# Performance work log

Measured on AMD Instinct MI355X. Metric: run time of the kernel, lower is better.

The kernel has to match this reference:

```python
import jax, jax.numpy as jnp
import numpy as np

C = 128          # multiplicity of 0e and 1o irreps
N = 16384        # number of tokens / points
SQRT2 = 2.0 ** 0.5
SQRT3 = 3.0 ** 0.5


def _tensor_square(s, v):
    """Per-channel symmetric tensor square of (1x0e + 1x1o).
    s: (N,C) scalars, v: (N,C,3) vectors.
    Returns ss:(N,C) 0e, sv:(N,C,3) 1o, vv0:(N,C) 0e, q:(N,C,5) 2e."""
    ss = s * s
    sv = SQRT2 * s[..., None] * v
    vv0 = jnp.sum(v * v, axis=-1) / SQRT3
    x, y, z = v[..., 0], v[..., 1], v[..., 2]
    q = jnp.stack([
        SQRT3 * x * y,
        SQRT3 * y * z,
        (2.0 * z * z - x * x - y * y) / 2.0,
        SQRT3 * x * z,
        SQRT3 * (x * x - y * y) / 2.0,
    ], axis=-1)
    return ss, sv, vv0, q


def _block(s, v, w1, w2, w0, wv):
    """_SelfInteractionBlock: tensor_square + concat/regroup + invariant-gated MLP + equivariant Linear."""
    ss, sv, vv0, q = _tensor_square(s, v)
    # regrouped features: 3C x 0e, 2C x 1o, C x 2e
    sc = jnp.concatenate([s, ss, vv0], axis=-1)            # (N, 3C)
    vec = jnp.concatenate([v, sv], axis=1)                 # (N, 2C, 3)
    # gate MLP on invariants (fan-in normalized, silu hidden)
    h = jax.nn.silu(sc @ w1 / jnp.sqrt(jnp.float32(sc.shape[-1])))
    g = h @ w2 / jnp.sqrt(jnp.float32(h.shape[-1]))        # (N, 6C) one gate per irrep
    g_s = g[:, :3 * C]
    g_v = g[:, 3 * C:5 * C]
    # (2e gates multiply q, which is dropped by the Linear to Cx0e+Cx1o)
    sc = sc * g_s
    vec = vec * g_v[..., None]
    # block-diagonal equivariant Linear -> C x 0e + C x 1o
    out_s = sc @ w0 / jnp.sqrt(jnp.float32(sc.shape[-1]))                      # (N, C)
    out_v = jnp.einsum('nmd,mc->ncd', vec, wv) / jnp.sqrt(jnp.float32(vec.shape[1]))  # (N, C, 3)
    return out_s, out_v


def _eq_layernorm(s, v, g0, g1, eps=1e-6):
    mu = jnp.mean(s, axis=-1, keepdims=True)
    sd = jnp.sqrt(jnp.mean((s - mu) ** 2, axis=-1, keepdims=True) + eps)
    s = (s - mu) / sd * g0
    rms = jnp.sqrt(jnp.mean(v * v, axis=(1, 2), keepdims=True) + eps)
    v = v / rms * g1[None, :, None]
    return s, v


def setup_inputs() -> dict:
    key = jax.random.key(0)
    ks = jax.random.split(key, 6)
    x = jax.random.normal(ks[0], (N, 4 * C), dtype=jnp.float32)
    mlp_w1 = jax.random.normal(ks[1], (2, 3 * C, 3 * C), dtype=jnp.float32)
    mlp_w2 = jax.random.normal(ks[2], (2, 3 * C, 6 * C), dtype=jnp.float32)
    lin_w0 = jax.random.normal(ks[3], (2, 3 * C, C), dtype=jnp.float32)
    lin_w1 = jax.random.normal(ks[4], (2, 2 * C, C), dtype=jnp.float32)
    ln_g0 = jnp.ones((C,), dtype=jnp.float32)
    ln_g1 = jnp.ones((C,), dtype=jnp.float32)
    return {"x": x, "mlp_w1": mlp_w1, "mlp_w2": mlp_w2,
            "lin_w0": lin_w0, "lin_w1": lin_w1, "ln_g0": ln_g0, "ln_g1": ln_g1}


def reference(x, mlp_w1, mlp_w2, lin_w0, lin_w1, ln_g0, ln_g1):
    n = x.shape[0]
    s = x[:, :C]                         # C x 0e
    v = x[:, C:].reshape(n, C, 3)        # C x 1o
    n_layers = mlp_w1.shape[0]
    for i in range(n_layers):
        ds, dv = _block(s, v, mlp_w1[i], mlp_w2[i], lin_w0[i], lin_w1[i])
        s = s + ds   # residual
        v = v + dv
        if i != n_layers - 1:  # norm on all but last layer (norm_last=False)
            s, v = _eq_layernorm(s, v, ln_g0, ln_g1)
    return jnp.concatenate([s, v.reshape(n, 3 * C)], axis=-1)
```

## Files before the change

### kernel.cpp

```cpp
#include <hip/hip_runtime.h>


typedef _Float16 half8 __attribute__((ext_vector_type(8)));
typedef float floatx4 __attribute__((ext_vector_type(4)));

static inline int cdiv_h(int a, int b){ return (a + b - 1) / b; }


__device__ __forceinline__ void stage16(const char* gaddr, char* lds_base){
  __builtin_amdgcn_global_load_lds((const __attribute__((address_space(1))) unsigned int*)gaddr,
                                   (__attribute__((address_space(3))) unsigned int*)lds_base,
                                   16, 0, 0);
}

__device__ __forceinline__ float wave_sum64(float x){
  #pragma unroll
  for (int m = 32; m; m >>= 1) x += __shfl_xor(x, m, 64);
  return x;
}

__device__ __forceinline__ void split_store(_Float16* p0, _Float16* p1, float v){
  _Float16 hi = (_Float16)v;
  *p0 = hi;
  *p1 = (_Float16)(v - (float)hi);
}

__device__ __forceinline__ unsigned int pack_split(float v){
  union { _Float16 h[2]; unsigned int u; } pk;
  _Float16 hi = (_Float16)v;
  pk.h[0] = hi;
  pk.h[1] = (_Float16)(v - (float)hi);
  return pk.u;
}

__device__ __forceinline__ void unzip16(uint4 p, uint2& hi, uint2& lo){
  hi.x = (p.x & 0xffffu) | (p.y << 16);
  hi.y = (p.z & 0xffffu) | (p.w << 16);
  lo.x = (p.x >> 16) | (p.y & 0xffff0000u);
  lo.y = (p.z >> 16) | (p.w & 0xffff0000u);
}

__device__ __forceinline__ void remap_xcd(int id, int nx, int ny, int& x, int& y){
  if (ny & 7){ x = id % nx; y = id / nx; return; }
  int xcd = id & 7, q = id >> 3, t = q / nx;
  x = q - t*nx; y = xcd + (t << 3);
}

__global__ __launch_bounds__(256) void prep_all(const float* __restrict__ w1,
                                                const float* __restrict__ w2,
                                                const float* __restrict__ w0,
                                                const float* __restrict__ wv,
                                                _Float16* __restrict__ W){
  const int PER_L = 475136;
  int idx = blockIdx.x*256 + threadIdx.x;
  if (idx >= 2*PER_L) return;
  int l = idx / PER_L;
  int r = idx - l*PER_L;
  const float RS384 = 0.051031036307982884f;
  _Float16* WL = W + (size_t)l*950272;
  const float* src; _Float16* dst; int K, ldw, col, k; float scale;
  if (r < 147456){
    src = w1 + (size_t)l*147456; dst = WL;            K = 384; ldw = 384; scale = RS384;
    col = r / 384; k = r - col*384;
  } else if (r < 393216){
    r -= 147456;
    src = w2 + (size_t)l*294912; dst = WL + 294912;   K = 384; ldw = 768; scale = RS384;
    col = r / 384; k = r - col*384;
  } else if (r < 442368){
    r -= 393216;
    src = w0 + (size_t)l*49152;  dst = WL + 786432;   K = 384; ldw = 128; scale = RS384;
    col = r / 384; k = r - col*384;
  } else {
    r -= 442368;
    src = wv + (size_t)l*32768;  dst = WL + 884736;   K = 256; ldw = 128; scale = 0.0625f;
    col = r / 256; k = r - col*256;
  }
  float v = src[(size_t)k*ldw + col] * scale;
  _Float16 hi = (_Float16)v;
  _Float16 lo = (_Float16)(v - (float)hi);
  size_t b = (size_t)col*2*K + k;
  dst[b]     = hi;
  dst[b + K] = lo;
}

__global__ __launch_bounds__(256) void e0_fused(const float* __restrict__ x,
                                                float* __restrict__ S,
                                                float* __restrict__ V,
                                                _Float16* __restrict__ A1,
                                                int row0){
  __shared__ alignas(16) float lx[4][512];
  const int n0 = blockIdx.x*4;
  const int tid = threadIdx.x;
  const float4* xs = (const float4*)(x + (size_t)(row0 + n0)*512);
  float4* ls = (float4*)(&lx[0][0]);
  ls[tid]       = xs[tid];
  ls[tid + 256] = xs[tid + 256];
  __syncthreads();
  const int w = tid >> 6, lane = tid & 63;
  const int n = n0 + w;
  const float* row = &lx[w][0];
  #pragma unroll
  for (int h = 0; h < 2; ++h){
    int ch = h*64 + lane;
    float s = row[ch];
    S[(size_t)n*128 + ch] = s;
    float vv = 0.f;
    #pragma unroll
    for (int d = 0; d < 3; ++d){
      float vd = row[128 + ch*3 + d];
      V[((size_t)n*3 + d)*128 + ch] = vd;
      vv += vd*vd;
    }
    float vals[3] = { s, s*s, vv * 0.5773502691896258f };
    #pragma unroll
    for (int q = 0; q < 3; ++q){
      size_t b = (size_t)n*768 + q*128 + ch;
      split_store(&A1[b], &A1[b + 384], vals[q]);
    }
  }
}

__global__ __launch_bounds__(256) void e3_fin(float* __restrict__ S, float* __restrict__ V,
                                              const float* __restrict__ OS, const float* __restrict__ OV,
                                              const float* __restrict__ g0, const float* __restrict__ g1,
                                              float* __restrict__ out, _Float16* __restrict__ A1,
                                              int row0, int doln){
  int n = blockIdx.x*4 + (threadIdx.x >> 6);
  int lane = threadIdx.x & 63;
  size_t sb = (size_t)n*128;
  size_t vb = (size_t)n*384;
  float s0 = S[sb + lane]      + OS[sb + lane];
  float s1 = S[sb + 64 + lane] + OS[sb + 64 + lane];
  float v[6];
  #pragma unroll
  for (int k = 0; k < 6; ++k) v[k] = V[vb + k*64 + lane] + OV[vb + k*64 + lane];

  if (doln){
    float mu = wave_sum64(s0 + s1) * (1.0f/128.0f);
    float d0 = s0 - mu, d1 = s1 - mu;
    float var = wave_sum64(d0*d0 + d1*d1) * (1.0f/128.0f);
    float sd = sqrtf(var + 1e-6f);
    float vvsum = 0.f;
    #pragma unroll
    for (int k = 0; k < 6; ++k) vvsum += v[k]*v[k];
    float rms = sqrtf(wave_sum64(vvsum) * (1.0f/384.0f) + 1e-6f);
    float s0n = d0 / sd * g0[lane];
    float s1n = d1 / sd * g0[64 + lane];
    S[sb + lane]      = s0n;
    S[sb + 64 + lane] = s1n;
    float vn[6];
    #pragma unroll
    for (int k = 0; k < 6; ++k){
      int j = k*64 + lane;
      vn[k] = v[k] / rms * g1[j & 127];
      V[vb + j] = vn[k];
    }
    float vv_a = vn[0]*vn[0] + vn[2]*vn[2] + vn[4]*vn[4];
    float vv_b = vn[1]*vn[1] + vn[3]*vn[3] + vn[5]*vn[5];
    float va[3] = { s0n, s0n*s0n, vv_a * 0.5773502691896258f };
    float vbv[3]= { s1n, s1n*s1n, vv_b * 0.5773502691896258f };
    #pragma unroll
    for (int q = 0; q < 3; ++q){
      size_t ba = (size_t)n*768 + q*128 + lane;
      split_store(&A1[ba], &A1[ba + 384], va[q]);
      size_t bb = ba + 64;
      split_store(&A1[bb], &A1[bb + 384], vbv[q]);
    }
  } else {
    size_t ob = (size_t)(row0 + n)*512;
    out[ob + lane]      = s0;
    out[ob + 64 + lane] = s1;
    #pragma unroll
    for (int k = 0; k < 6; ++k){
      int j = k*64 + lane;
      int d = j >> 7, ch = j & 127;
      out[ob + 128 + ch*3 + d] = v[k];
    }
  }
}

__device__ __forceinline__ void gemm_mainloop(const _Float16* __restrict__ A,
                                              const _Float16* __restrict__ BT,
                                              int lda, int kbase, int m0, int c0,
                                              _Float16 (&ls)[2][12288],
                                              floatx4 (&acc)[4][2]){
  const int nsc  = kbase >> 5;
  const int ldbt = 2*kbase;
  const int tid  = threadIdx.x;
  const int wave = tid >> 6, lane = tid & 63;
  const int wm = wave & 1, wn = wave >> 1;
  const int r = lane & 15, kg = lane >> 4;
  const int slot = kg ^ ((r >> 1) & 3);

  auto stage = [&](int c, int buf){
    const int ka = c << 5;
    char* lb = (char*)(&ls[buf][0]);
    #pragma unroll
    for (int p = 0; p < 2; ++p){
      const int lbase = wave*1024 + p*4096;
      const int off = lbase + lane*16;
      const int row = off >> 6;
      const int bir = (off & 63) ^ (((off >> 7) & 3) << 4);
      const char* gah = (const char*)A + (((size_t)(m0 + row))*lda + ka)*2 + bir;
      stage16(gah, lb + lbase);
      const char* gal = (const char*)A + (((size_t)(m0 + row))*lda + kbase + ka)*2 + bir;
      stage16(gal, lb + 8192 + lbase);
    }
    {
      const int lbase = wave*1024;
      const int off = lbase + lane*16;
      const int row = off >> 6;
      const int bir = (off & 63) ^ (((off >> 7) & 3) << 4);
      const char* gbh = (const char*)BT + (((size_t)(c0 + row))*ldbt + ka)*2 + bir;
      stage16(gbh, lb + 16384 + lbase);
      const char* gbl = (const char*)BT + (((size_t)(c0 + row))*ldbt + kbase + ka)*2 + bir;
      stage16(gbl, lb + 20480 + lbase);
    }
  };

  stage(0, 0);
  for (int c = 0; c < nsc; ++c){
    __syncthreads();
    if (c + 1 < nsc) stage(c + 1, (c + 1) & 1);
    const char* base = (const char*)&ls[c & 1][0];
    half8 ah[4], al[4], bh[2], bl[2];
    #pragma unroll
    for (int mt = 0; mt < 4; ++mt){
      const int ro = (wm*64 + mt*16 + r)*64 + slot*16;
      ah[mt] = *(const half8*)(base + ro);
      al[mt] = *(const half8*)(base + 8192 + ro);
    }
    #pragma unroll
    for (int nt = 0; nt < 2; ++nt){
      const int ro = (wn*32 + nt*16 + r)*64 + slot*16;
      bh[nt] = *(const half8*)(base + 16384 + ro);
      bl[nt] = *(const half8*)(base + 20480 + ro);
    }
    #pragma unroll
    for (int mt = 0; mt < 4; ++mt)
      #pragma unroll
      for (int nt = 0; nt < 2; ++nt)
        acc[mt][nt] = __builtin_amdgcn_mfma_f32_16x16x32_f16(ah[mt], bh[nt], acc[mt][nt], 0, 0, 0);
    #pragma unroll
    for (int mt = 0; mt < 4; ++mt)
      #pragma unroll
      for (int nt = 0; nt < 2; ++nt)
        acc[mt][nt] = __builtin_amdgcn_mfma_f32_16x16x32_f16(ah[mt], bl[nt], acc[mt][nt], 0, 0, 0);
    #pragma unroll
    for (int mt = 0; mt < 4; ++mt)
      #pragma unroll
      for (int nt = 0; nt < 2; ++nt)
        acc[mt][nt] = __builtin_amdgcn_mfma_f32_16x16x32_f16(al[mt], bh[nt], acc[mt][nt], 0, 0, 0);
  }
}

template<int MODE>
__global__ __launch_bounds__(256, 3) void gemm_split(const _Float16* __restrict__ A,
                                                     const _Float16* __restrict__ BT,
                                                     _Float16* __restrict__ OUT,
                                                     const float* __restrict__ S,
                                                     const float* __restrict__ V,
                                                     _Float16* __restrict__ A1g,
                                                     _Float16* __restrict__ A4,
                                                     int lda, int kbase, int nx, int ny){
  __shared__ alignas(16) _Float16 ls[2][12288];
  int bx, by; remap_xcd(blockIdx.x, nx, ny, bx, by);
  const int c0 = bx << 6, m0 = by << 7;
  floatx4 acc[4][2];
  #pragma unroll
  for (int i = 0; i < 4; ++i)
    #pragma unroll
    for (int j = 0; j < 2; ++j) acc[i][j] = (floatx4){0.f, 0.f, 0.f, 0.f};

  gemm_mainloop(A, BT, lda, kbase, m0, c0, ls, acc);

  const int tid = threadIdx.x;
  const int wave = tid >> 6, lane = tid & 63;
  const int wm = wave & 1, wn = wave >> 1;
  const int r = lane & 15, kg = lane >> 4;
  char* scr = (char*)&ls[0][0];

  if (MODE == 1){
    #pragma unroll
    for (int h = 0; h < 2; ++h){
      __syncthreads();
      if (wm == h){
        #pragma unroll
        for (int mt = 0; mt < 4; ++mt)
          #pragma unroll
          for (int nt = 0; nt < 2; ++nt)
            #pragma unroll
            for (int i = 0; i < 4; ++i){
              int rl = mt*16 + kg*4 + i;
              int cl = wn*32 + nt*16 + r;
              int pc = cl ^ (kg << 4);
              float g = acc[mt][nt][i];
              float hh = g / (1.0f + __expf(-g));
              *(unsigned int*)(scr + rl*256 + pc*4) = pack_split(hh);
            }
      }
      __syncthreads();
      #pragma unroll 1
      for (int j = 0; j < 4; ++j){
        int lin = j*256 + tid, rl = lin >> 4, seg = lin & 15;
        int cs = seg ^ (((rl >> 2) & 3) << 2);
        uint4 p = *(const uint4*)(scr + rl*256 + cs*16);
        uint2 hi, lo; unzip16(p, hi, lo);
        _Float16* rowp = OUT + (size_t)(m0 + h*64 + rl)*768 + c0 + seg*4;
        *(uint2*)rowp         = hi;
        *(uint2*)(rowp + 384) = lo;
      }
    }
  } else if (c0 < 384){
    #pragma unroll
    for (int h = 0; h < 2; ++h){
      __syncthreads();
      #pragma unroll 1
      for (int j = 0; j < 2; ++j){
        int lin = j*256 + tid, rl = lin >> 3, seg = lin & 7;
        int cs = seg ^ (((rl >> 2) & 3) << 1);
        const _Float16* gp = A1g + (size_t)(m0 + h*64 + rl)*768 + c0 + seg*8;
        *(float4*)(scr + rl*128 + cs*16)        = *(const float4*)gp;
        *(float4*)(scr + 8192 + rl*128 + cs*16) = *(const float4*)(gp + 384);
      }
      __syncthreads();
      if (wm == h){
        #pragma unroll
        for (int mt = 0; mt < 4; ++mt)
          #pragma unroll
          for (int nt = 0; nt < 2; ++nt)
            #pragma unroll
            for (int i = 0; i < 4; ++i){
              int rl = mt*16 + kg*4 + i;
              int cl = wn*32 + nt*16 + r;
              int pc = cl ^ (kg << 4);
              _Float16* phi = (_Float16*)scr + rl*64 + pc;
              _Float16* plo = (_Float16*)(scr + 8192) + rl*64 + pc;
              float sc = (float)*phi + (float)*plo;
              split_store(phi, plo, sc * acc[mt][nt][i]);
            }
      }
      __syncthreads();
      #pragma unroll 1
      for (int j = 0; j < 2; ++j){
        int lin = j*256 + tid, rl = lin >> 3, seg = lin & 7;
        int cs = seg ^ (((rl >> 2) & 3) << 1);
        _Float16* gp = A1g + (size_t)(m0 + h*64 + rl)*768 + c0 + seg*8;
        *(float4*)gp         = *(const float4*)(scr + rl*128 + cs*16);
        *(float4*)(gp + 384) = *(const float4*)(scr + 8192 + rl*128 + cs*16);
      }
    }
  } else {
    const int mm0 = c0 - 384;
    const int ch0 = mm0 & 127;
    if (mm0 >= 128){
      #pragma unroll
      for (int mt = 0; mt < 4; ++mt)
        #pragma unroll
        for (int nt = 0; nt < 2; ++nt)
          #pragma unroll
          for (int i = 0; i < 4; ++i){
            int row = m0 + wm*64 + mt*16 + kg*4 + i;
            int cl  = wn*32 + nt*16 + r;
            acc[mt][nt][i] *= 1.4142135623730951f * S[(size_t)row*128 + ch0 + cl];
          }
    }
    for (int d = 0; d < 3; ++d){
      #pragma unroll
      for (int h = 0; h < 2; ++h){
        __syncthreads();
        #pragma unroll 1
        for (int j = 0; j < 4; ++j){
          int lin = j*256 + tid, rl = lin >> 4, seg = lin & 15;
          int cs = seg ^ (((rl >> 2) & 3) << 2);
          *(float4*)(scr + rl*256 + cs*16) =
            *(const float4*)(V + ((size_t)(m0 + h*64 + rl)*3 + d)*128 + ch0 + seg*4);
        }
        __syncthreads();
        if (wm == h){
          #pragma unroll
          for (int mt = 0; mt < 4; ++mt)
            #pragma unroll
            for (int nt = 0; nt < 2; ++nt)
              #pragma unroll
              for (int i = 0; i < 4; ++i){
                int rl = mt*16 + kg*4 + i;
                int cl = wn*32 + nt*16 + r;
                int pc = cl ^ (kg << 4);
                float* pw = (float*)(scr + rl*256) + pc;
                *(unsigned int*)pw = pack_split(*pw * acc[mt][nt][i]);
              }
        }
        __syncthreads();
        #pragma unroll 1
        for (int j = 0; j < 4; ++j){
          int lin = j*256 + tid, rl = lin >> 4, seg = lin & 15;
          int cs = seg ^ (((rl >> 2) & 3) << 2);
          uint4 p = *(const uint4*)(scr + rl*256 + cs*16);
          uint2 hi, lo; unzip16(p, hi, lo);
          _Float16* rowp = A4 + ((size_t)(m0 + h*64 + rl)*3 + d)*512 + mm0 + seg*4;
          *(uint2*)rowp         = hi;
          *(uint2*)(rowp + 256) = lo;
        }
      }
    }
  }
}

__global__ __launch_bounds__(256, 3) void gemm_pair(const _Float16* __restrict__ Aa,
                                                    const _Float16* __restrict__ Ba,
                                                    float* __restrict__ Ca, int ny0,
                                                    const _Float16* __restrict__ Ab,
                                                    const _Float16* __restrict__ Bb,
                                                    float* __restrict__ Cb, int ny1){
  __shared__ alignas(16) _Float16 ls[2][12288];
  const _Float16 *A, *BT; float* C; int lda, kbase, bx, by;
  const int id = blockIdx.x;
  if (id < 2*ny0){
    remap_xcd(id, 2, ny0, bx, by);
    A = Aa; BT = Ba; C = Ca; lda = 768; kbase = 384;
  } else {
    remap_xcd(id - 2*ny0, 2, ny1, bx, by);
    A = Ab; BT = Bb; C = Cb; lda = 512; kbase = 256;
  }
  const int c0 = bx << 6, m0 = by << 7;
  floatx4 acc[4][2];
  #pragma unroll
  for (int i = 0; i < 4; ++i)
    #pragma unroll
    for (int j = 0; j < 2; ++j) acc[i][j] = (floatx4){0.f, 0.f, 0.f, 0.f};

  gemm_mainloop(A, BT, lda, kbase, m0, c0, ls, acc);

  const int wave = threadIdx.x >> 6, lane = threadIdx.x & 63;
  const int wm = wave & 1, wn = wave >> 1;
  const int r = lane & 15, kg = lane >> 4;
  #pragma unroll
  for (int mt = 0; mt < 4; ++mt)
    #pragma unroll
    for (int nt = 0; nt < 2; ++nt)
      #pragma unroll
      for (int i = 0; i < 4; ++i){
        const int row = m0 + wm*64 + mt*16 + kg*4 + i;
        const int col = c0 + wn*32 + nt*16 + r;
        C[(size_t)row*128 + col] = acc[mt][nt][i];
      }
}


extern "C" void kernel_launch(void* const* d_in, const int* in_sizes, int n_in,
                              void* d_out, int out_size, void* d_ws, size_t ws_size,
                              hipStream_t stream){
  const float* x  = (const float*)d_in[0];
  const float* w1 = (const float*)d_in[1];
  const float* w2 = (const float*)d_in[2];
  const float* w0 = (const float*)d_in[3];
  const float* wv = (const float*)d_in[4];
  const float* g0 = (const float*)d_in[5];
  const float* g1 = (const float*)d_in[6];
  float* out = (float*)d_out;
  const int N = in_sizes[0] / 512;

  const size_t HL = 950272;
  _Float16* W = (_Float16*)d_ws;
  const size_t wbytes = 2*HL*2;

  int cnum = 128;
  for (int cc = 1; cc <= 128; cc <<= 1){
    size_t need = wbytes + (size_t)(N/cc)*10240;
    if (need <= ws_size){ cnum = cc; break; }
  }
  const int R = N / cnum;
  const int ny = R / 128;

  char* p = (char*)d_ws + wbytes;
  float*    Sst = (float*)p;     p += (size_t)R*512;
  float*    Vst = (float*)p;     p += (size_t)R*1536;
  _Float16* A1  = (_Float16*)p;  p += (size_t)R*1536;
  _Float16* A2  = (_Float16*)p;  p += (size_t)R*1536;
  _Float16* A4  = (_Float16*)p;  p += (size_t)R*3072;
  float*    OS  = (float*)p;     p += (size_t)R*512;
  float*    OV  = (float*)p;     p += (size_t)R*1536;

  prep_all<<<cdiv_h(2*475136,256),256,0,stream>>>(w1, w2, w0, wv, W);

  for (int chk = 0; chk < cnum; ++chk){
    const int row0 = chk*R;
    e0_fused<<<R/4,256,0,stream>>>(x, Sst, Vst, A1, row0);
    for (int l = 0; l < 2; ++l){
      _Float16* W1p = W + (size_t)l*HL;
      _Float16* W2p = W1p + 294912;
      _Float16* W0p = W1p + 786432;
      _Float16* WVp = W1p + 884736;
      gemm_split<1><<<6*ny,256,0,stream>>>(A1, W1p, A2,
          nullptr, nullptr, nullptr, nullptr, 768, 384, 6, ny);
      gemm_split<2><<<10*ny,256,0,stream>>>(A2, W2p, nullptr,
          Sst, Vst, A1, A4, 768, 384, 10, ny);
      gemm_pair<<<8*ny,256,0,stream>>>(A1, W0p, OS, ny, A4, WVp, OV, 3*ny);
      e3_fin<<<R/4,256,0,stream>>>(Sst, Vst, OS, OV, g0, g1, out, A1, row0, (l == 0) ? 1 : 0);
    }
  }
}
```

Baseline: 357.4 us.

## Load GEMM operands directly from global memory into registers, dropping LDS staging

Replaces the double-buffered global_load_lds staging of A/B tiles in shared memory with direct per-lane 16-byte global loads into MFMA operand registers. This removes LDS traffic and the per-iteration __syncthreads. The epilogue scratch shrinks to 16 KB, and launch bounds go from 3 to 4 blocks per SM for more occupancy. The cost is that each wave now reloads data the other waves also use, so there is no intra-block reuse and global/L2 traffic rises. With no prefetch, load latency is exposed at every k-step.

```diff
diff --git a/kernel.cpp b/kernel.cpp
--- a/kernel.cpp
+++ b/kernel.cpp
@@ -6,12 +6,6 @@
 
 static inline int cdiv_h(int a, int b){ return (a + b - 1) / b; }
 
-
-__device__ __forceinline__ void stage16(const char* gaddr, char* lds_base){
-  __builtin_amdgcn_global_load_lds((const __attribute__((address_space(1))) unsigned int*)gaddr,
-                                   (__attribute__((address_space(3))) unsigned int*)lds_base,
-                                   16, 0, 0);
-}
 
 __device__ __forceinline__ float wave_sum64(float x){
   #pragma unroll
@@ -182,60 +176,30 @@
 __device__ __forceinline__ void gemm_mainloop(const _Float16* __restrict__ A,
                                               const _Float16* __restrict__ BT,
                                               int lda, int kbase, int m0, int c0,
-                                              _Float16 (&ls)[2][12288],
                                               floatx4 (&acc)[4][2]){
-  const int nsc  = kbase >> 5;
+  const int nsc = kbase >> 5;
   const int ldbt = 2*kbase;
-  const int tid  = threadIdx.x;
+  const int tid = threadIdx.x;
   const int wave = tid >> 6, lane = tid & 63;
   const int wm = wave & 1, wn = wave >> 1;
   const int r = lane & 15, kg = lane >> 4;
-  const int slot = kg ^ ((r >> 1) & 3);
-
-  auto stage = [&](int c, int buf){
-    const int ka = c << 5;
-    char* lb = (char*)(&ls[buf][0]);
-    #pragma unroll
-    for (int p = 0; p < 2; ++p){
-      const int lbase = wave*1024 + p*4096;
-      const int off = lbase + lane*16;
-      const int row = off >> 6;
-      const int bir = (off & 63) ^ (((off >> 7) & 3) << 4);
-      const char* gah = (const char*)A + (((size_t)(m0 + row))*lda + ka)*2 + bir;
-      stage16(gah, lb + lbase);
-      const char* gal = (const char*)A + (((size_t)(m0 + row))*lda + kbase + ka)*2 + bir;
-      stage16(gal, lb + 8192 + lbase);
-    }
-    {
-      const int lbase = wave*1024;
-      const int off = lbase + lane*16;
-      const int row = off >> 6;
-      const int bir = (off & 63) ^ (((off >> 7) & 3) << 4);
-      const char* gbh = (const char*)BT + (((size_t)(c0 + row))*ldbt + ka)*2 + bir;
-      stage16(gbh, lb + 16384 + lbase);
-      const char* gbl = (const char*)BT + (((size_t)(c0 + row))*ldbt + kbase + ka)*2 + bir;
-      stage16(gbl, lb + 20480 + lbase);
-    }
-  };
-
-  stage(0, 0);
+
+  const _Float16* pa0 = A + (size_t)(m0 + wm*64 +  0 + r)*lda + kg*8;
+  const _Float16* pa1 = A + (size_t)(m0 + wm*64 + 16 + r)*lda + kg*8;
+  const _Float16* pa2 = A + (size_t)(m0 + wm*64 + 32 + r)*lda + kg*8;
+  const _Float16* pa3 = A + (size_t)(m0 + wm*64 + 48 + r)*lda + kg*8;
+  const _Float16* pb0 = BT + (size_t)(c0 + wn*32 +  0 + r)*ldbt + kg*8;
+  const _Float16* pb1 = BT + (size_t)(c0 + wn*32 + 16 + r)*ldbt + kg*8;
+
   for (int c = 0; c < nsc; ++c){
-    __syncthreads();
-    if (c + 1 < nsc) stage(c + 1, (c + 1) & 1);
-    const char* base = (const char*)&ls[c & 1][0];
     half8 ah[4], al[4], bh[2], bl[2];
-    #pragma unroll
-    for (int mt = 0; mt < 4; ++mt){
-      const int ro = (wm*64 + mt*16 + r)*64 + slot*16;
-      ah[mt] = *(const half8*)(base + ro);
-      al[mt] = *(const half8*)(base + 8192 + ro);
-    }
-    #pragma unroll
-    for (int nt = 0; nt < 2; ++nt){
-      const int ro = (wn*32 + nt*16 + r)*64 + slot*16;
-      bh[nt] = *(const half8*)(base + 16384 + ro);
-      bl[nt] = *(const half8*)(base + 20480 + ro);
-    }
+    ah[0] = *(const half8*)pa0;  al[0] = *(const half8*)(pa0 + kbase);
+    ah[1] = *(const half8*)pa1;  al[1] = *(const half8*)(pa1 + kbase);
+    ah[2] = *(const half8*)pa2;  al[2] = *(const half8*)(pa2 + kbase);
+    ah[3] = *(const half8*)pa3;  al[3] = *(const half8*)(pa3 + kbase);
+    bh[0] = *(const half8*)pb0;  bl[0] = *(const half8*)(pb0 + kbase);
+    bh[1] = *(const half8*)pb1;  bl[1] = *(const half8*)(pb1 + kbase);
+    pa0 += 32; pa1 += 32; pa2 += 32; pa3 += 32; pb0 += 32; pb1 += 32;
     #pragma unroll
     for (int mt = 0; mt < 4; ++mt)
       #pragma unroll
@@ -255,7 +219,7 @@
 }
 
 template<int MODE>
-__global__ __launch_bounds__(256, 3) void gemm_split(const _Float16* __restrict__ A,
+__global__ __launch_bounds__(256, 4) void gemm_split(const _Float16* __restrict__ A,
                                                      const _Float16* __restrict__ BT,
                                                      _Float16* __restrict__ OUT,
                                                      const float* __restrict__ S,
@@ -263,7 +227,7 @@
                                                      _Float16* __restrict__ A1g,
                                                      _Float16* __restrict__ A4,
                                                      int lda, int kbase, int nx, int ny){
-  __shared__ alignas(16) _Float16 ls[2][12288];
+  __shared__ alignas(16) char scr[16384];
   int bx, by; remap_xcd(blockIdx.x, nx, ny, bx, by);
   const int c0 = bx << 6, m0 = by << 7;
   floatx4 acc[4][2];
@@ -272,13 +236,12 @@
     #pragma unroll
     for (int j = 0; j < 2; ++j) acc[i][j] = (floatx4){0.f, 0.f, 0.f, 0.f};
 
-  gemm_mainloop(A, BT, lda, kbase, m0, c0, ls, acc);
+  gemm_mainloop(A, BT, lda, kbase, m0, c0, acc);
 
   const int tid = threadIdx.x;
   const int wave = tid >> 6, lane = tid & 63;
   const int wm = wave & 1, wn = wave >> 1;
   const int r = lane & 15, kg = lane >> 4;
-  char* scr = (char*)&ls[0][0];
 
   if (MODE == 1){
     #pragma unroll
@@ -407,13 +370,12 @@
   }
 }
 
-__global__ __launch_bounds__(256, 3) void gemm_pair(const _Float16* __restrict__ Aa,
+__global__ __launch_bounds__(256, 4) void gemm_pair(const _Float16* __restrict__ Aa,
                                                     const _Float16* __restrict__ Ba,
                                                     float* __restrict__ Ca, int ny0,
                                                     const _Float16* __restrict__ Ab,
                                                     const _Float16* __restrict__ Bb,
                                                     float* __restrict__ Cb, int ny1){
-  __shared__ alignas(16) _Float16 ls[2][12288];
   const _Float16 *A, *BT; float* C; int lda, kbase, bx, by;
   const int id = blockIdx.x;
   if (id < 2*ny0){
@@ -430,7 +392,7 @@
     #pragma unroll
     for (int j = 0; j < 2; ++j) acc[i][j] = (floatx4){0.f, 0.f, 0.f, 0.f};
 
-  gemm_mainloop(A, BT, lda, kbase, m0, c0, ls, acc);
+  gemm_mainloop(A, BT, lda, kbase, m0, c0, acc);
 
   const int wave = threadIdx.x >> 6, lane = threadIdx.x & 63;
   const int wm = wave & 1, wn = wave >> 1;
```

Measured after the change: 564.0 us. +57.8%, slower.
